# Optimization experiments

Measured on AMD Instinct MI355X. Metric: run time of the kernel, lower is better.

Reference implementation:

```python
import jax, jax.numpy as jnp
import numpy as np

B, C, H, W = 8, 3, 1024, 1024
N_SPOTS = int(H * W * 0.015)  # 15728, matches torch: n = int(H*W*0.015)
KSIZE, SIGMA = 5, 1.5
RMAX = 3  # max snow-box radius (torch.randint(1, 4))


def setup_inputs() -> dict:
    key = jax.random.key(0)
    k1, k2, k3, k4 = jax.random.split(key, 4)
    x = jax.random.uniform(k1, (B, C, H, W), dtype=jnp.float32)
    ys = jax.random.randint(k2, (B, N_SPOTS), 0, H)
    xs = jax.random.randint(k3, (B, N_SPOTS), 0, W)
    rs = jax.random.randint(k4, (B, N_SPOTS), 0, 3)  # radius = rs + 1 in {1,2,3}
    return {"x": x, "ys": ys, "xs": xs, "rs": rs}


def _snow_mask(ys, xs, rs, h, w):
    # Union of axis-aligned boxes: pixel (py,px) is snow iff some spot has
    # |py - y| <= r and |px - x| <= r (box clipping to the image is equivalent).
    b, n = ys.shape
    r = rs + 1  # radii 1..3
    d = jnp.arange(-RMAX, RMAX + 1)
    dy = jnp.repeat(d, 2 * RMAX + 1)  # [49]
    dx = jnp.tile(d, 2 * RMAX + 1)    # [49]
    yy = ys[:, :, None] + dy  # [B, n, 49]
    xx = xs[:, :, None] + dx
    valid = ((jnp.abs(dy) <= r[:, :, None]) & (jnp.abs(dx) <= r[:, :, None])
             & (yy >= 0) & (yy < h) & (xx >= 0) & (xx < w))
    yy = jnp.where(valid, yy, h)  # out-of-bounds sentinel -> dropped by scatter
    xx = jnp.where(valid, xx, w)
    b_idx = jnp.broadcast_to(jnp.arange(b)[:, None, None], yy.shape)
    mask = jnp.zeros((b, h, w), dtype=bool)
    mask = mask.at[b_idx, yy, xx].set(True, mode="drop")
    return mask


def _gauss_kernel():
    coords = jnp.arange(KSIZE, dtype=jnp.float32) - KSIZE // 2
    g = jnp.exp(-coords ** 2 / (2.0 * SIGMA ** 2))
    g = g / g.sum()
    return jnp.outer(g, g)  # [5, 5]


def reference(x, ys, xs, rs):
    b, c, h, w = x.shape
    mask = _snow_mask(ys, xs, rs, h, w)                   # [B, H, W]
    out = jnp.where(mask[:, None, :, :], jnp.float32(0.95), x)
    kernel = jnp.broadcast_to(_gauss_kernel(), (c, 1, KSIZE, KSIZE))  # depthwise OIHW
    pad = KSIZE // 2
    out = jax.lax.conv_general_dilated(
        out, kernel, window_strides=(1, 1), padding=[(pad, pad), (pad, pad)],
        dimension_numbers=("NCHW", "OIHW", "NCHW"), feature_group_count=c)
    return jnp.clip(out, 0.0, 1.0)
```

## Files before the change

### kernel.cpp

```cpp
#include <hip/hip_runtime.h>

#define BB 8
#define CC 3
#define HH 1024
#define WW 1024
#define NS 15728

#define G0 0.1200784f
#define G1 0.2338808f
#define G2 0.2920816f

__global__ __launch_bounds__(256) void snow_mask_kernel(
    const int* __restrict__ ys, const int* __restrict__ xs,
    const int* __restrict__ rs, unsigned int* __restrict__ mbits) {
  int s = blockIdx.x * 256 + threadIdx.x;
  if (s >= NS) return;
  int b = blockIdx.y;
  int idx = b * NS + s;
  int y = ys[idx];
  int x = xs[idx];
  int r = rs[idx] + 1;
  int x0 = max(x - r, 0), x1 = min(x + r, WW - 1);
  int y0 = max(y - r, 0), y1 = min(y + r, HH - 1);
  int w0 = x0 >> 5, w1 = x1 >> 5;
  unsigned int m0 = 0xFFFFFFFFu << (x0 & 31);
  unsigned int m1 = 0xFFFFFFFFu >> (31 - (x1 & 31));
  for (int py = y0; py <= y1; ++py) {
    unsigned int* rowp = mbits + ((unsigned)(b * HH + py) << 5);
    if (w0 == w1) {
      atomicOr(&rowp[w0], m0 & m1);
    } else {
      atomicOr(&rowp[w0], m0);
      atomicOr(&rowp[w1], m1);
    }
  }
}

#define TS 140
#define NLOAD 2312

__global__ __launch_bounds__(256, 4) void snow_blur_kernel(
    const float* __restrict__ x, const unsigned int* __restrict__ mbits,
    float* __restrict__ out) {
  __shared__ float tile[68 * TS];

  const int bz = blockIdx.z;
  const int b = bz / CC;
  const int bx = blockIdx.x, by = blockIdx.y;
  const int tid = threadIdx.x;
  const float* __restrict__ xp = x + (size_t)bz * (HH * WW);
  const unsigned int* __restrict__ mb = mbits + ((unsigned)(b * HH) << 5);

  const int gxbase = bx * 128 - 4;
  const int gybase = by * 64 - 2;

  float4 v[10];
  unsigned int bits[10];
  int lidx[10];
#pragma unroll
  for (int k = 0; k < 10; ++k) {
    int i = tid + k * 256;
    i = i < (NLOAD - 1) ? i : (NLOAD - 1);
    int r = i / 34;
    int c4 = i - r * 34;
    int gy = gybase + r;
    int gx = gxbase + c4 * 4;
    int gyc = min(max(gy, 0), HH - 1);
    int gxc = min(max(gx, 0), WW - 4);
    v[k] = *(const float4*)(xp + (size_t)gyc * WW + gxc);
    unsigned int bm = (mb[(gyc << 5) + (gxc >> 5)] >> (gxc & 31)) & 0xFu;
    if ((gy != gyc) | (gx != gxc)) bm = 16u;
    bits[k] = bm;
    lidx[k] = r * TS + c4 * 4;
  }
#pragma unroll
  for (int k = 0; k < 10; ++k) {
    float4 t = v[k];
    unsigned int bm = bits[k];
    if (bm & 1u) t.x = 0.95f;
    if (bm & 2u) t.y = 0.95f;
    if (bm & 4u) t.z = 0.95f;
    if (bm & 8u) t.w = 0.95f;
    if (bm & 16u) { t.x = 0.f; t.y = 0.f; t.z = 0.f; t.w = 0.f; }
    *(float4*)&tile[lidx[k]] = t;
  }
  __syncthreads();

  const int c = tid & 31;
  const int ty = tid >> 5;
  const float* trow = tile + (ty * 8) * TS + c * 4;

  auto hrow = [&](int j, float4& h) {
    const float* p = trow + j * TS;
    float4 A = *(const float4*)(p);
    float4 Bv = *(const float4*)(p + 4);
    float2 Cv = *(const float2*)(p + 8);
    h.x = G0 * (A.z + Bv.z) + G1 * (A.w + Bv.y) + G2 * Bv.x;
    h.y = G0 * (A.w + Bv.w) + G1 * (Bv.x + Bv.z) + G2 * Bv.y;
    h.z = G0 * (Bv.x + Cv.x) + G1 * (Bv.y + Bv.w) + G2 * Bv.z;
    h.w = G0 * (Bv.y + Cv.y) + G1 * (Bv.z + Cv.x) + G2 * Bv.w;
  };

  float4 h0, h1, h2, h3, h4;
  hrow(0, h0); hrow(1, h1); hrow(2, h2); hrow(3, h3); hrow(4, h4);

  float* op = out + (size_t)bz * (HH * WW) +
              (size_t)(by * 64 + ty * 8) * WW + (bx * 128 + c * 4);
#pragma unroll
  for (int k = 0; k < 8; ++k) {
    float4 s;
    s.x = G0 * (h0.x + h4.x) + G1 * (h1.x + h3.x) + G2 * h2.x;
    s.y = G0 * (h0.y + h4.y) + G1 * (h1.y + h3.y) + G2 * h2.y;
    s.z = G0 * (h0.z + h4.z) + G1 * (h1.z + h3.z) + G2 * h2.z;
    s.w = G0 * (h0.w + h4.w) + G1 * (h1.w + h3.w) + G2 * h2.w;
    s.x = fminf(fmaxf(s.x, 0.f), 1.f);
    s.y = fminf(fmaxf(s.y, 0.f), 1.f);
    s.z = fminf(fmaxf(s.z, 0.f), 1.f);
    s.w = fminf(fmaxf(s.w, 0.f), 1.f);
    *(float4*)op = s;
    op += WW;
    h0 = h1; h1 = h2; h2 = h3; h3 = h4;
    if (k < 7) hrow(k + 5, h4);
  }
}

extern "C" void kernel_launch(void* const* d_in, const int* in_sizes, int n_in,
                              void* d_out, int out_size, void* d_ws, size_t ws_size,
                              hipStream_t stream) {
  const float* x = (const float*)d_in[0];
  const int* ys = (const int*)d_in[1];
  const int* xs = (const int*)d_in[2];
  const int* rs = (const int*)d_in[3];
  float* out = (float*)d_out;

  unsigned int* mbits = (unsigned int*)d_ws;
  hipMemsetAsync(mbits, 0, (size_t)BB * HH * WW / 8, stream);

  dim3 mgrid((NS + 255) / 256, BB);
  snow_mask_kernel<<<mgrid, 256, 0, stream>>>(ys, xs, rs, mbits);

  dim3 grid(WW / 128, HH / 64, BB * CC);
  snow_blur_kernel<<<grid, 256, 0, stream>>>(x, mbits, out);
}
```

Baseline: 210.2 us.

## Replace shared-memory tile blur with full-row register strip streaming

```diff
diff --git a/kernel.cpp b/kernel.cpp
--- a/kernel.cpp
+++ b/kernel.cpp
@@ -36,91 +36,112 @@
   }
 }
 
-#define TS 140
-#define NLOAD 2312
+#define STRIP 32
+
+struct Row {
+  float4 v;
+  float2 lh, rh;
+  unsigned int m0, m1;
+};
+
+__device__ __forceinline__ Row load_row(const float* __restrict__ xrow,
+                                        const unsigned int* __restrict__ mrow,
+                                        int off_v, int off_l, int off_r,
+                                        int iw0, int iw1) {
+  Row rd;
+  rd.v = *(const float4*)(xrow + off_v);
+  rd.lh = *(const float2*)(xrow + off_l);
+  rd.rh = *(const float2*)(xrow + off_r);
+  rd.m0 = mrow[iw0];
+  rd.m1 = mrow[iw1];
+  return rd;
+}
+
+__device__ __forceinline__ float4 hpass(Row rd, int bitpos,
+                                        bool l_edge, bool r_edge, bool valid) {
+  unsigned long long mm =
+      (unsigned long long)rd.m0 | ((unsigned long long)rd.m1 << 32);
+  unsigned int bits = (unsigned int)(mm >> bitpos);
+  float4 v = rd.v;
+  float2 lh = rd.lh, rh = rd.rh;
+  if (bits & 1u)   lh.x = 0.95f;
+  if (bits & 2u)   lh.y = 0.95f;
+  if (bits & 4u)   v.x = 0.95f;
+  if (bits & 8u)   v.y = 0.95f;
+  if (bits & 16u)  v.z = 0.95f;
+  if (bits & 32u)  v.w = 0.95f;
+  if (bits & 64u)  rh.x = 0.95f;
+  if (bits & 128u) rh.y = 0.95f;
+  if (l_edge) { lh.x = 0.f; lh.y = 0.f; }
+  if (r_edge) { rh.x = 0.f; rh.y = 0.f; }
+  float4 h;
+  h.x = G0 * (lh.x + v.z) + G1 * (lh.y + v.y) + G2 * v.x;
+  h.y = G0 * (lh.y + v.w) + G1 * (v.x + v.z) + G2 * v.y;
+  h.z = G0 * (v.x + rh.x) + G1 * (v.y + v.w) + G2 * v.z;
+  h.w = G0 * (v.y + rh.y) + G1 * (v.z + rh.x) + G2 * v.w;
+  if (!valid) { h.x = 0.f; h.y = 0.f; h.z = 0.f; h.w = 0.f; }
+  return h;
+}
 
 __global__ __launch_bounds__(256, 4) void snow_blur_kernel(
     const float* __restrict__ x, const unsigned int* __restrict__ mbits,
     float* __restrict__ out) {
-  __shared__ float tile[68 * TS];
-
-  const int bz = blockIdx.z;
+  const int bz = blockIdx.y;
   const int b = bz / CC;
-  const int bx = blockIdx.x, by = blockIdx.y;
-  const int tid = threadIdx.x;
+  const int gy0 = blockIdx.x * STRIP;
+  const int t = threadIdx.x;
   const float* __restrict__ xp = x + (size_t)bz * (HH * WW);
   const unsigned int* __restrict__ mb = mbits + ((unsigned)(b * HH) << 5);
 
-  const int gxbase = bx * 128 - 4;
-  const int gybase = by * 64 - 2;
-
-  float4 v[10];
-  unsigned int bits[10];
-  int lidx[10];
-#pragma unroll
-  for (int k = 0; k < 10; ++k) {
-    int i = tid + k * 256;
-    i = i < (NLOAD - 1) ? i : (NLOAD - 1);
-    int r = i / 34;
-    int c4 = i - r * 34;
-    int gy = gybase + r;
-    int gx = gxbase + c4 * 4;
-    int gyc = min(max(gy, 0), HH - 1);
-    int gxc = min(max(gx, 0), WW - 4);
-    v[k] = *(const float4*)(xp + (size_t)gyc * WW + gxc);
-    unsigned int bm = (mb[(gyc << 5) + (gxc >> 5)] >> (gxc & 31)) & 0xFu;
-    if ((gy != gyc) | (gx != gxc)) bm = 16u;
-    bits[k] = bm;
-    lidx[k] = r * TS + c4 * 4;
-  }
-#pragma unroll
-  for (int k = 0; k < 10; ++k) {
-    float4 t = v[k];
-    unsigned int bm = bits[k];
-    if (bm & 1u) t.x = 0.95f;
-    if (bm & 2u) t.y = 0.95f;
-    if (bm & 4u) t.z = 0.95f;
-    if (bm & 8u) t.w = 0.95f;
-    if (bm & 16u) { t.x = 0.f; t.y = 0.f; t.z = 0.f; t.w = 0.f; }
-    *(float4*)&tile[lidx[k]] = t;
-  }
-  __syncthreads();
-
-  const int c = tid & 31;
-  const int ty = tid >> 5;
-  const float* trow = tile + (ty * 8) * TS + c * 4;
-
-  auto hrow = [&](int j, float4& h) {
-    const float* p = trow + j * TS;
-    float4 A = *(const float4*)(p);
-    float4 Bv = *(const float4*)(p + 4);
-    float2 Cv = *(const float2*)(p + 8);
-    h.x = G0 * (A.z + Bv.z) + G1 * (A.w + Bv.y) + G2 * Bv.x;
-    h.y = G0 * (A.w + Bv.w) + G1 * (Bv.x + Bv.z) + G2 * Bv.y;
-    h.z = G0 * (Bv.x + Cv.x) + G1 * (Bv.y + Bv.w) + G2 * Bv.z;
-    h.w = G0 * (Bv.y + Cv.y) + G1 * (Bv.z + Cv.x) + G2 * Bv.w;
-  };
+  const int c = 4 * t;
+  const int off_v = c;
+  const int off_l = max(c - 2, 0);
+  const int off_r = min(c + 4, WW - 2);
+  const int iw0 = max((c - 2) >> 5, 0);
+  const int iw1 = min((c + 4) >> 5, 31);
+  const int bitpos = (c - 2) & 31;
+  const bool l_edge = (t == 0);
+  const bool r_edge = (t == 255);
 
   float4 h0, h1, h2, h3, h4;
-  hrow(0, h0); hrow(1, h1); hrow(2, h2); hrow(3, h3); hrow(4, h4);
+  h0 = h1 = h2 = h3 = make_float4(0.f, 0.f, 0.f, 0.f);
+  (void)h0;
 
-  float* op = out + (size_t)bz * (HH * WW) +
-              (size_t)(by * 64 + ty * 8) * WW + (bx * 128 + c * 4);
+  int ir0 = gy0 - 2;
+  int g0c = min(max(ir0, 0), HH - 1);
+  Row cur = load_row(xp + (size_t)g0c * WW, mb + (g0c << 5),
+                     off_v, off_l, off_r, iw0, iw1);
+
+  float* op = out + (size_t)bz * (HH * WW) + (size_t)gy0 * WW + c;
+
 #pragma unroll
-  for (int k = 0; k < 8; ++k) {
-    float4 s;
-    s.x = G0 * (h0.x + h4.x) + G1 * (h1.x + h3.x) + G2 * h2.x;
-    s.y = G0 * (h0.y + h4.y) + G1 * (h1.y + h3.y) + G2 * h2.y;
-    s.z = G0 * (h0.z + h4.z) + G1 * (h1.z + h3.z) + G2 * h2.z;
-    s.w = G0 * (h0.w + h4.w) + G1 * (h1.w + h3.w) + G2 * h2.w;
-    s.x = fminf(fmaxf(s.x, 0.f), 1.f);
-    s.y = fminf(fmaxf(s.y, 0.f), 1.f);
-    s.z = fminf(fmaxf(s.z, 0.f), 1.f);
-    s.w = fminf(fmaxf(s.w, 0.f), 1.f);
-    *(float4*)op = s;
-    op += WW;
-    h0 = h1; h1 = h2; h2 = h3; h3 = h4;
-    if (k < 7) hrow(k + 5, h4);
+  for (int r = 0; r < STRIP + 4; ++r) {
+    int ir = gy0 - 2 + r;
+    bool valid = (ir >= 0) && (ir < HH);
+
+    Row nxt;
+    if (r < STRIP + 3) {
+      int g2 = min(max(ir + 1, 0), HH - 1);
+      nxt = load_row(xp + (size_t)g2 * WW, mb + (g2 << 5),
+                     off_v, off_l, off_r, iw0, iw1);
+    }
+
+    float4 hh = hpass(cur, bitpos, l_edge, r_edge, valid);
+    h0 = h1; h1 = h2; h2 = h3; h3 = h4; h4 = hh;
+
+    if (r >= 4) {
+      float4 s;
+      s.x = G0 * (h0.x + h4.x) + G1 * (h1.x + h3.x) + G2 * h2.x;
+      s.y = G0 * (h0.y + h4.y) + G1 * (h1.y + h3.y) + G2 * h2.y;
+      s.z = G0 * (h0.z + h4.z) + G1 * (h1.z + h3.z) + G2 * h2.z;
+      s.w = G0 * (h0.w + h4.w) + G1 * (h1.w + h3.w) + G2 * h2.w;
+      s.x = fminf(fmaxf(s.x, 0.f), 1.f);
+      s.y = fminf(fmaxf(s.y, 0.f), 1.f);
+      s.z = fminf(fmaxf(s.z, 0.f), 1.f);
+      s.w = fminf(fmaxf(s.w, 0.f), 1.f);
+      *(float4*)(op + (size_t)(r - 4) * WW) = s;
+    }
+    cur = nxt;
   }
 }
 
@@ -139,6 +160,6 @@
   dim3 mgrid((NS + 255) / 256, BB);
   snow_mask_kernel<<<mgrid, 256, 0, stream>>>(ys, xs, rs, mbits);
 
-  dim3 grid(WW / 128, HH / 64, BB * CC);
+  dim3 grid(HH / STRIP, BB * CC);
   snow_blur_kernel<<<grid, 256, 0, stream>>>(x, mbits, out);
 }
```

Result: slower. 218.7 us (+4.1%).
